# Kernel tuning notes

Measured on AMD Instinct MI355X. Metric: run time of the kernel, lower is better.

## Reference

```python
import jax, jax.numpy as jnp
import numpy as np

B, S, E, H, R = 2, 1024, 1024, 16, 32
D = E // H  # head_dim = 64


def setup_inputs() -> dict:
    key = jax.random.key(0)
    ks = jax.random.split(key, 8)
    f = jax.random.normal
    return {
        "query": f(ks[0], (B, S, E), jnp.float32),
        "key": f(ks[1], (B, S, E), jnp.float32),  # unused by the module's forward, kept for signature fidelity
        "value": f(ks[2], (B, S, E), jnp.float32),
        "rules_keys": f(ks[3], (H, R, D), jnp.float32) * 0.02,   # nn.init.normal_(std=0.02)
        "rules_widths": jnp.ones((H, R, D), jnp.float32),
        "Wq": f(ks[4], (E, E), jnp.float32) * (E ** -0.5),
        "bq": jnp.zeros((E,), jnp.float32),
        "Wv": f(ks[5], (E * R, E), jnp.float32) * (E ** -0.5),
        "bv": jnp.zeros((E * R,), jnp.float32),
        "Wo": f(ks[6], (E, E), jnp.float32) * (E ** -0.5),
        "bo": jnp.zeros((E,), jnp.float32),
    }


def reference(query, key, value, rules_keys, rules_widths, Wq, bq, Wv, bv, Wo, bo):
    scale = D ** -0.5
    # query projection -> per-head layout (B,S,H,D)
    q = ((query @ Wq.T) + bq) * scale
    q = q.reshape(B, S, H, D)
    # fuzzy Gaussian membership: L1 distance to rule keys, scaled by widths,
    # HTSK -> mean over head_dim. z: (B,S,H,R)
    diff = jnp.abs(q[:, :, :, None, :] - rules_keys[None, None])        # (B,S,H,R,D)
    z = -0.5 * jnp.mean((diff / rules_widths[None, None]) ** 2, axis=-1)  # (B,S,H,R)
    attn = jax.nn.softmax(z, axis=-1)  # softmax over rules (dropout p=0 -> identity)
    # value projection to per-rule values: (B,S,H,R,D)
    v = ((value @ Wv.T) + bv) * scale
    v = v.reshape(B, S, H, D, R).transpose(0, 1, 2, 4, 3)
    # rule-weighted aggregation
    out = jnp.einsum('bshr,bshrd->bshd', attn, v)  # (B,S,H,D)
    # faithful to original torch code: transpose(1,2) then view(B,-1,H*D)
    # (this is a head-major flatten, reproduced exactly)
    out = out.transpose(0, 2, 1, 3).reshape(B, S, H * D)
    return (out @ Wo.T) + bo
```

## Files before the change

### kernel.cpp

```cpp
#include <hip/hip_runtime.h>
#include <hip/hip_bf16.h>
#include <cstdint>

typedef float f32x4 __attribute__((ext_vector_type(4)));
typedef short bf16x8 __attribute__((ext_vector_type(8)));

__device__ __forceinline__ unsigned short f32_to_bf16_rne(float f) {
  unsigned int u = __float_as_uint(f);
  return (unsigned short)((u + 0x7FFFu + ((u >> 16) & 1u)) >> 16);
}

#define GLOAD_LDS16(gptr, lptr)                                                             \
  __builtin_amdgcn_global_load_lds((const __attribute__((address_space(1))) unsigned int*)(gptr), \
                                   (__attribute__((address_space(3))) unsigned int*)(lptr), 16, 0, 0)

__global__ __launch_bounds__(256) void cvt_all(const float* __restrict__ wv,
                                               const float* __restrict__ q,
                                               const float* __restrict__ v,
                                               const float* __restrict__ wq,
                                               const float* __restrict__ wo,
                                               unsigned short* __restrict__ wvb,
                                               unsigned short* __restrict__ qb,
                                               unsigned short* __restrict__ vb,
                                               unsigned short* __restrict__ wqb,
                                               unsigned short* __restrict__ wob) {
  int i = blockIdx.x * 256 + threadIdx.x;
  const float* src;
  unsigned short* dst;
  int off;
  if (i < 4194304)      { src = wv; dst = wvb; off = i; }
  else if (i < 4456448) { src = q;  dst = qb;  off = i - 4194304; }
  else if (i < 4718592) { src = v;  dst = vb;  off = i - 4456448; }
  else if (i < 4849664) { src = wq; dst = wqb; off = i - 4718592; }
  else                  { src = wo; dst = wob; off = i - 4849664; }
  const float4* s = (const float4*)src;
  float4 a = s[2 * off], b = s[2 * off + 1];
  uint4 o;
  o.x = (unsigned)f32_to_bf16_rne(a.x) | ((unsigned)f32_to_bf16_rne(a.y) << 16);
  o.y = (unsigned)f32_to_bf16_rne(a.z) | ((unsigned)f32_to_bf16_rne(a.w) << 16);
  o.z = (unsigned)f32_to_bf16_rne(b.x) | ((unsigned)f32_to_bf16_rne(b.y) << 16);
  o.w = (unsigned)f32_to_bf16_rne(b.z) | ((unsigned)f32_to_bf16_rne(b.w) << 16);
  ((uint4*)dst)[off] = o;
}

__global__ __launch_bounds__(256) void fuzzy2_k(const float* __restrict__ qf,
                                                const float* __restrict__ rk,
                                                const float* __restrict__ rw,
                                                float* __restrict__ attn) {
  __shared__ float lk[32][65];
  __shared__ float lc[32][65];
  const int tid = threadIdx.x;
  const int h = blockIdx.y;
  const int mbase = blockIdx.x * 128;

  for (int idx = tid; idx < 2048; idx += 256) {
    int r = idx >> 6, d = idx & 63;
    lk[r][d] = rk[(size_t)(h * 32 + r) * 64 + d];
    float w = rw[(size_t)(h * 32 + r) * 64 + d];
    lc[r][d] = 0.0078125f / (w * w);
  }
  __syncthreads();

  const int g = tid >> 5;
  const int r = tid & 31;
#pragma unroll 1
  for (int it = 0; it < 16; ++it) {
    int m = mbase + it * 8 + g;
    const float* qrow = qf + (size_t)m * 1024 + h * 64;
    float acc = 0.f;
#pragma unroll
    for (int d0 = 0; d0 < 64; d0 += 4) {
      float4 q4 = *(const float4*)(qrow + d0);
      const float* qp = (const float*)&q4;
#pragma unroll
      for (int j = 0; j < 4; ++j) {
        float diff = qp[j] - lk[r][d0 + j];
        acc += lc[r][d0 + j] * diff * diff;
      }
    }
    float z = -acc;
    float mx = z;
#pragma unroll
    for (int mask = 16; mask >= 1; mask >>= 1) mx = fmaxf(mx, __shfl_xor(mx, mask));
    float e = __expf(z - mx);
    float s = e;
#pragma unroll
    for (int mask = 16; mask >= 1; mask >>= 1) s += __shfl_xor(s, mask);
    attn[(size_t)m * 512 + h * 32 + r] = e / s;
  }
}

__global__ __launch_bounds__(256) void gemm_bt64(const unsigned short* __restrict__ A,
                                                 const unsigned short* __restrict__ W,
                                                 const float* __restrict__ bias, float scale,
                                                 int M, int N, int K, float* __restrict__ Cf) {
  constexpr int BK = 32;
  __shared__ unsigned short As[2][64 * BK];
  __shared__ unsigned short Bs[2][64 * BK];
  const int tid = threadIdx.x;
  const int wid = tid >> 6;
  const int lane = tid & 63;
  const int l15 = lane & 15;
  const int l4 = lane >> 4;
  const int bm = blockIdx.y * 64;
  const int bn = blockIdx.x * 64;
  const int wr = (wid >> 1) * 32;
  const int wc = (wid & 1) * 32;

  f32x4 acc[2][2];
#pragma unroll
  for (int i = 0; i < 2; ++i)
#pragma unroll
    for (int j = 0; j < 2; ++j) acc[i][j] = (f32x4){0.f, 0.f, 0.f, 0.f};

  const int nk = K / BK;
  auto stage = [&](int buf, int kt) {
    int c = tid;
    int row = c >> 2, ch = c & 3;
    int sch = ch ^ ((row >> 1) & 3);
    GLOAD_LDS16(A + (size_t)(bm + row) * K + kt * BK + sch * 8, &As[buf][c * 8]);
    GLOAD_LDS16(W + (size_t)(bn + row) * K + kt * BK + sch * 8, &Bs[buf][c * 8]);
  };

  stage(0, 0);
  __syncthreads();

  for (int kt = 0; kt < nk; ++kt) {
    const int cur = kt & 1;
    if (kt + 1 < nk) stage(cur ^ 1, kt + 1);
    bf16x8 a[2], b[2];
#pragma unroll
    for (int mi = 0; mi < 2; ++mi) {
      int rl = wr + mi * 16 + l15;
      int ph = (rl * 64 + l4 * 16) ^ ((((unsigned)rl >> 1) & 3) << 4);
      a[mi] = *(const bf16x8*)((const char*)&As[cur][0] + ph);
    }
#pragma unroll
    for (int ni = 0; ni < 2; ++ni) {
      int rl = wc + ni * 16 + l15;
      int ph = (rl * 64 + l4 * 16) ^ ((((unsigned)rl >> 1) & 3) << 4);
      b[ni] = *(const bf16x8*)((const char*)&Bs[cur][0] + ph);
    }
#pragma unroll
    for (int mi = 0; mi < 2; ++mi)
#pragma unroll
      for (int ni = 0; ni < 2; ++ni)
        acc[mi][ni] = __builtin_amdgcn_mfma_f32_16x16x32_bf16(a[mi], b[ni], acc[mi][ni], 0, 0, 0);
    __syncthreads();
  }

#pragma unroll
  for (int mi = 0; mi < 2; ++mi) {
#pragma unroll
    for (int ni = 0; ni < 2; ++ni) {
      int gm = bm + wr + mi * 16 + l4 * 4;
      int gn = bn + wc + ni * 16 + l15;
      float bval = bias[gn];
#pragma unroll
      for (int q = 0; q < 4; ++q)
        Cf[(size_t)(gm + q) * N + gn] = (acc[mi][ni][q] + bval) * scale;
    }
  }
}

__global__ __launch_bounds__(512, 4) void gemm2_k(const unsigned short* __restrict__ A,
                                                  const unsigned short* __restrict__ W,
                                                  const float* __restrict__ bias, float scale,
                                                  const float* __restrict__ attn,
                                                  unsigned short* __restrict__ X) {
  constexpr int K = 1024, BK = 32, NK = K / BK;
  extern __shared__ unsigned short lds[];
  unsigned short* Asl = lds;
  unsigned short* Bsl = lds + 3 * 4096;
  const int tid = threadIdx.x;
  const int wid = tid >> 6, lane = tid & 63;
  const int l15 = lane & 15, l4 = lane >> 4;
  const int wm = wid >> 2, wn = wid & 3;

  int orig = blockIdx.x;
  int swz = (orig & 7) * 256 + (orig >> 3);
  const int bm = (swz & 15) * 128, bn = (swz >> 4) * 256;

  auto stageA = [&](int buf, int kt) {
    int c = tid;
    int row = c >> 2, ch = c & 3;
    int sch = ch ^ ((row >> 1) & 3);
    GLOAD_LDS16(A + (size_t)(bm + row) * K + kt * BK + sch * 8, Asl + buf * 4096 + c * 8);
  };
  auto stageB = [&](int buf, int kt) {
#pragma unroll
    for (int i = 0; i < 2; ++i) {
      int c = i * 512 + tid;
      int row = c >> 2, ch = c & 3;
      int sch = ch ^ ((row >> 1) & 3);
      GLOAD_LDS16(W + (size_t)(bn + row) * K + kt * BK + sch * 8, Bsl + buf * 8192 + c * 8);
    }
  };

  f32x4 acc[4][4];
#pragma unroll
  for (int i = 0; i < 4; ++i)
#pragma unroll
    for (int j = 0; j < 4; ++j) acc[i][j] = (f32x4){0.f, 0.f, 0.f, 0.f};

  bf16x8 a[4], b[4];

#define FRAG_PH(rl) (((rl) * 64 + l4 * 16) ^ ((((unsigned)(rl) >> 1) & 3) << 4))

#define BODY(CUR, NXT, STG, Tt, DO_STAGE, WN)                                             \
  do {                                                                                    \
    if (DO_STAGE) { stageA(STG, (Tt) + 2); stageB(STG, (Tt) + 2); }                       \
    asm volatile("s_waitcnt vmcnt(" #WN ")" ::: "memory");                                \
    __builtin_amdgcn_s_barrier();                                                         \
    {                                                                                     \
      const char* _ab = (const char*)(Asl + (NXT) * 4096);                                \
      const char* _bb = (const char*)(Bsl + (NXT) * 8192);                                \
      __builtin_amdgcn_s_setprio(1);                                                      \
      _Pragma("unroll") for (int mf = 0; mf < 4; ++mf) {                                  \
        _Pragma("unroll") for (int nf = 0; nf < 4; ++nf) {                                \
          acc[mf][nf] =                                                                   \
              __builtin_amdgcn_mfma_f32_16x16x32_bf16(a[mf], b[nf], acc[mf][nf], 0, 0, 0);\
          if (mf == 3) {                                                                  \
            int rl = wn * 64 + nf * 16 + l15;                                             \
            b[nf] = *(const bf16x8*)(_bb + FRAG_PH(rl));                                  \
          }                                                                               \
        }                                                                                 \
        int rl = wm * 64 + mf * 16 + l15;                                                 \
        a[mf] = *(const bf16x8*)(_ab + FRAG_PH(rl));                                      \
      }                                                                                   \
      __builtin_amdgcn_s_setprio(0);                                                      \
    }                                                                                     \
    asm volatile("s_waitcnt lgkmcnt(0)" ::: "memory");                                    \
    __builtin_amdgcn_sched_barrier(0);                                                    \
  } while (0)

  stageA(0, 0); stageB(0, 0);
  stageA(1, 1); stageB(1, 1);
  asm volatile("s_waitcnt vmcnt(3)" ::: "memory");
  __builtin_amdgcn_s_barrier();
#pragma unroll
  for (int nf = 0; nf < 4; ++nf) {
    int rl = wn * 64 + nf * 16 + l15;
    b[nf] = *(const bf16x8*)((const char*)Bsl + FRAG_PH(rl));
  }
#pragma unroll
  for (int mf = 0; mf < 4; ++mf) {
    int rl = wm * 64 + mf * 16 + l15;
    a[mf] = *(const bf16x8*)((const char*)Asl + FRAG_PH(rl));
  }
  asm volatile("s_waitcnt lgkmcnt(0)" ::: "memory");
  __builtin_amdgcn_sched_barrier(0);

  for (int T = 0; T < 30; T += 3) {
    BODY(0, 1, 2, T, 1, 3);
    BODY(1, 2, 0, (T + 1), 1, 3);
    BODY(2, 0, 1, (T + 2), 1, 3);
  }
  BODY(0, 1, 2, 30, 0, 0);
  __builtin_amdgcn_s_setprio(1);
#pragma unroll
  for (int mf = 0; mf < 4; ++mf)
#pragma unroll
    for (int nf = 0; nf < 4; ++nf)
      acc[mf][nf] = __builtin_amdgcn_mfma_f32_16x16x32_bf16(a[mf], b[nf], acc[mf][nf], 0, 0, 0);
  __builtin_amdgcn_s_setprio(0);
#undef BODY
#undef FRAG_PH

  const int h = bn >> 11;
  const int dbase = ((bn & 2047) + wn * 64) >> 5;
#pragma unroll
  for (int mf = 0; mf < 4; ++mf) {
    int gm0 = bm + wm * 64 + mf * 16 + l4 * 4;
    float red[4][2];
#pragma unroll
    for (int q = 0; q < 4; ++q) { red[q][0] = 0.f; red[q][1] = 0.f; }
#pragma unroll
    for (int nf = 0; nf < 4; ++nf) {
      int col = bn + wn * 64 + nf * 16 + l15;
      float bval = bias[col];
      int r = (nf & 1) * 16 + l15;
      int g = nf >> 1;
#pragma unroll
      for (int q = 0; q < 4; ++q) {
        float w = attn[(size_t)(gm0 + q) * 512 + h * 32 + r];
        red[q][g] += (acc[mf][nf][q] + bval) * w;
      }
    }
#pragma unroll
    for (int q = 0; q < 4; ++q)
#pragma unroll
      for (int g = 0; g < 2; ++g) {
        float vv = red[q][g];
        for (int mask = 1; mask < 16; mask <<= 1) vv += __shfl_xor(vv, mask);
        red[q][g] = vv * scale;
      }
    if (l15 == 0) {
#pragma unroll
      for (int q = 0; q < 4; ++q) {
        int m = gm0 + q;
        int bb = m >> 10, s = m & 1023;
        size_t base = (((size_t)(bb * 16 + h)) * 1024 + s) * 64;
        unsigned lo = f32_to_bf16_rne(red[q][0]);
        unsigned hi = f32_to_bf16_rne(red[q][1]);
        ((unsigned*)X)[(base + dbase) >> 1] = lo | (hi << 16);
      }
    }
  }
}

extern "C" void kernel_launch(void* const* d_in, const int* in_sizes, int n_in, void* d_out,
                              int out_size, void* d_ws, size_t ws_size, hipStream_t stream) {
  const float* query = (const float*)d_in[0];
  const float* value = (const float*)d_in[2];
  const float* rk = (const float*)d_in[3];
  const float* rw = (const float*)d_in[4];
  const float* Wq = (const float*)d_in[5];
  const float* bq = (const float*)d_in[6];
  const float* Wv = (const float*)d_in[7];
  const float* bv = (const float*)d_in[8];
  const float* Wo = (const float*)d_in[9];
  const float* bo = (const float*)d_in[10];
  float* out = (float*)d_out;

  const float scale = 0.125f;

  char* p = (char*)d_ws;
  unsigned short* Wv_b = (unsigned short*)p; p += (size_t)33554432 * 2;
  unsigned short* Aq_b = (unsigned short*)p; p += (size_t)2097152 * 2;
  unsigned short* Av_b = (unsigned short*)p; p += (size_t)2097152 * 2;
  unsigned short* Wq_b = (unsigned short*)p; p += (size_t)1048576 * 2;
  unsigned short* Wo_b = (unsigned short*)p; p += (size_t)1048576 * 2;
  float* qf = (float*)p;   p += (size_t)2097152 * 4;
  float* attn = (float*)p; p += (size_t)1048576 * 4;
  unsigned short* X = (unsigned short*)p;

  cvt_all<<<19456, 256, 0, stream>>>(Wv, query, value, Wq, Wo, Wv_b, Aq_b, Av_b, Wq_b, Wo_b);

  gemm_bt64<<<dim3(16, 32), 256, 0, stream>>>(Aq_b, Wq_b, bq, scale, 2048, 1024, 1024, qf);
  fuzzy2_k<<<dim3(16, 16), 256, 0, stream>>>(qf, rk, rw, attn);
  hipFuncSetAttribute((const void*)gemm2_k, hipFuncAttributeMaxDynamicSharedMemorySize, 73728);
  gemm2_k<<<2048, 512, 73728, stream>>>(Av_b, Wv_b, bv, scale, attn, X);
  gemm_bt64<<<dim3(16, 32), 256, 0, stream>>>(X, Wo_b, bo, 1.0f, 2048, 1024, 1024, out);
}
```

Before: 235.2 us.

## Enlarge gemm2 tile to 256x256 with 4-stage LDS ring and double-buffered fragments

```diff
diff --git a/kernel.cpp b/kernel.cpp
--- a/kernel.cpp
+++ b/kernel.cpp
@@ -163,29 +163,32 @@
   }
 }
 
-__global__ __launch_bounds__(512, 4) void gemm2_k(const unsigned short* __restrict__ A,
-                                                  const unsigned short* __restrict__ W,
-                                                  const float* __restrict__ bias, float scale,
-                                                  const float* __restrict__ attn,
-                                                  unsigned short* __restrict__ X) {
+__global__ __launch_bounds__(512) void gemm2_k(const unsigned short* __restrict__ A,
+                                               const unsigned short* __restrict__ W,
+                                               const float* __restrict__ bias, float scale,
+                                               const float* __restrict__ attn,
+                                               unsigned short* __restrict__ X) {
   constexpr int K = 1024, BK = 32, NK = K / BK;
   extern __shared__ unsigned short lds[];
   unsigned short* Asl = lds;
-  unsigned short* Bsl = lds + 3 * 4096;
+  unsigned short* Bsl = lds + 4 * 8192;
   const int tid = threadIdx.x;
   const int wid = tid >> 6, lane = tid & 63;
   const int l15 = lane & 15, l4 = lane >> 4;
   const int wm = wid >> 2, wn = wid & 3;
 
   int orig = blockIdx.x;
-  int swz = (orig & 7) * 256 + (orig >> 3);
-  const int bm = (swz & 15) * 128, bn = (swz >> 4) * 256;
+  int swz = (orig & 7) * 128 + (orig >> 3);
+  const int bm = (swz & 7) * 256, bn = (swz >> 3) * 256;
 
   auto stageA = [&](int buf, int kt) {
-    int c = tid;
-    int row = c >> 2, ch = c & 3;
-    int sch = ch ^ ((row >> 1) & 3);
-    GLOAD_LDS16(A + (size_t)(bm + row) * K + kt * BK + sch * 8, Asl + buf * 4096 + c * 8);
+#pragma unroll
+    for (int i = 0; i < 2; ++i) {
+      int c = i * 512 + tid;
+      int row = c >> 2, ch = c & 3;
+      int sch = ch ^ ((row >> 1) & 3);
+      GLOAD_LDS16(A + (size_t)(bm + row) * K + kt * BK + sch * 8, Asl + buf * 8192 + c * 8);
+    }
   };
   auto stageB = [&](int buf, int kt) {
 #pragma unroll
@@ -197,36 +200,37 @@
     }
   };
 
-  f32x4 acc[4][4];
-#pragma unroll
-  for (int i = 0; i < 4; ++i)
+  f32x4 acc[8][4];
+#pragma unroll
+  for (int i = 0; i < 8; ++i)
 #pragma unroll
     for (int j = 0; j < 4; ++j) acc[i][j] = (f32x4){0.f, 0.f, 0.f, 0.f};
 
-  bf16x8 a[4], b[4];
+  bf16x8 a0[8], a1[8], b0[4], b1[4];
 
 #define FRAG_PH(rl) (((rl) * 64 + l4 * 16) ^ ((((unsigned)(rl) >> 1) & 3) << 4))
 
-#define BODY(CUR, NXT, STG, Tt, DO_STAGE, WN)                                             \
+#define BODY(aC, aN, bC, bN, Tt, DO_STAGE, WN)                                            \
   do {                                                                                    \
-    if (DO_STAGE) { stageA(STG, (Tt) + 2); stageB(STG, (Tt) + 2); }                       \
+    if (DO_STAGE) { stageA(((Tt) + 2) & 3, (Tt) + 2); stageB(((Tt) + 2) & 3, (Tt) + 2); } \
     asm volatile("s_waitcnt vmcnt(" #WN ")" ::: "memory");                                \
     __builtin_amdgcn_s_barrier();                                                         \
     {                                                                                     \
-      const char* _ab = (const char*)(Asl + (NXT) * 4096);                                \
-      const char* _bb = (const char*)(Bsl + (NXT) * 8192);                                \
+      const char* _ab = (const char*)(Asl + (((Tt) + 1) & 3) * 8192);                     \
+      const char* _bb = (const char*)(Bsl + (((Tt) + 1) & 3) * 8192);                     \
       __builtin_amdgcn_s_setprio(1);                                                      \
-      _Pragma("unroll") for (int mf = 0; mf < 4; ++mf) {                                  \
-        _Pragma("unroll") for (int nf = 0; nf < 4; ++nf) {                                \
+      _Pragma("unroll") for (int mf = 0; mf < 8; ++mf) {                                  \
+        _Pragma("unroll") for (int nf = 0; nf < 4; ++nf)                                  \
           acc[mf][nf] =                                                                   \
-              __builtin_amdgcn_mfma_f32_16x16x32_bf16(a[mf], b[nf], acc[mf][nf], 0, 0, 0);\
-          if (mf == 3) {                                                                  \
-            int rl = wn * 64 + nf * 16 + l15;                                             \
-            b[nf] = *(const bf16x8*)(_bb + FRAG_PH(rl));                                  \
-          }                                                                               \
+              __builtin_amdgcn_mfma_f32_16x16x32_bf16(aC[mf], bC[nf], acc[mf][nf], 0, 0, 0); \
+        if (mf < 4) {                                                                     \
+          aN[mf] = *(const bf16x8*)(_ab + FRAG_PH(wm * 128 + mf * 16 + l15));             \
+          bN[mf] = *(const bf16x8*)(_bb + FRAG_PH(wn * 64 + mf * 16 + l15));              \
+        } else if (mf < 6) {                                                              \
+          int i0 = 2 * mf - 4, i1 = 2 * mf - 3;                                           \
+          aN[i0] = *(const bf16x8*)(_ab + FRAG_PH(wm * 128 + i0 * 16 + l15));             \
+          aN[i1] = *(const bf16x8*)(_ab + FRAG_PH(wm * 128 + i1 * 16 + l15));             \
         }                                                                                 \
-        int rl = wm * 64 + mf * 16 + l15;                                                 \
-        a[mf] = *(const bf16x8*)(_ab + FRAG_PH(rl));                                      \
       }                                                                                   \
       __builtin_amdgcn_s_setprio(0);                                                      \
     }                                                                                     \
@@ -236,33 +240,28 @@
 
   stageA(0, 0); stageB(0, 0);
   stageA(1, 1); stageB(1, 1);
-  asm volatile("s_waitcnt vmcnt(3)" ::: "memory");
+  asm volatile("s_waitcnt vmcnt(4)" ::: "memory");
   __builtin_amdgcn_s_barrier();
 #pragma unroll
-  for (int nf = 0; nf < 4; ++nf) {
-    int rl = wn * 64 + nf * 16 + l15;
-    b[nf] = *(const bf16x8*)((const char*)Bsl + FRAG_PH(rl));
-  }
-#pragma unroll
-  for (int mf = 0; mf < 4; ++mf) {
-    int rl = wm * 64 + mf * 16 + l15;
-    a[mf] = *(const bf16x8*)((const char*)Asl + FRAG_PH(rl));
-  }
+  for (int nf = 0; nf < 4; ++nf)
+    b0[nf] = *(const bf16x8*)((const char*)Bsl + FRAG_PH(wn * 64 + nf * 16 + l15));
+#pragma unroll
+  for (int mf = 0; mf < 8; ++mf)
+    a0[mf] = *(const bf16x8*)((const char*)Asl + FRAG_PH(wm * 128 + mf * 16 + l15));
   asm volatile("s_waitcnt lgkmcnt(0)" ::: "memory");
   __builtin_amdgcn_sched_barrier(0);
 
-  for (int T = 0; T < 30; T += 3) {
-    BODY(0, 1, 2, T, 1, 3);
-    BODY(1, 2, 0, (T + 1), 1, 3);
-    BODY(2, 0, 1, (T + 2), 1, 3);
-  }
-  BODY(0, 1, 2, 30, 0, 0);
+  for (int T = 0; T < 30; T += 2) {
+    BODY(a0, a1, b0, b1, T, 1, 4);
+    BODY(a1, a0, b1, b0, (T + 1), 1, 4);
+  }
+  BODY(a0, a1, b0, b1, 30, 0, 0);
   __builtin_amdgcn_s_setprio(1);
 #pragma unroll
-  for (int mf = 0; mf < 4; ++mf)
+  for (int mf = 0; mf < 8; ++mf)
 #pragma unroll
     for (int nf = 0; nf < 4; ++nf)
-      acc[mf][nf] = __builtin_amdgcn_mfma_f32_16x16x32_bf16(a[mf], b[nf], acc[mf][nf], 0, 0, 0);
+      acc[mf][nf] = __builtin_amdgcn_mfma_f32_16x16x32_bf16(a1[mf], b1[nf], acc[mf][nf], 0, 0, 0);
   __builtin_amdgcn_s_setprio(0);
 #undef BODY
 #undef FRAG_PH
@@ -270,8 +269,8 @@
   const int h = bn >> 11;
   const int dbase = ((bn & 2047) + wn * 64) >> 5;
 #pragma unroll
-  for (int mf = 0; mf < 4; ++mf) {
-    int gm0 = bm + wm * 64 + mf * 16 + l4 * 4;
+  for (int mf = 0; mf < 8; ++mf) {
+    int gm0 = bm + wm * 128 + mf * 16 + l4 * 4;
     float red[4][2];
 #pragma unroll
     for (int q = 0; q < 4; ++q) { red[q][0] = 0.f; red[q][1] = 0.f; }
@@ -339,7 +338,7 @@
 
   gemm_bt64<<<dim3(16, 32), 256, 0, stream>>>(Aq_b, Wq_b, bq, scale, 2048, 1024, 1024, qf);
   fuzzy2_k<<<dim3(16, 16), 256, 0, stream>>>(qf, rk, rw, attn);
-  hipFuncSetAttribute((const void*)gemm2_k, hipFuncAttributeMaxDynamicSharedMemorySize, 73728);
-  gemm2_k<<<2048, 512, 73728, stream>>>(Av_b, Wv_b, bv, scale, attn, X);
+  hipFuncSetAttribute((const void*)gemm2_k, hipFuncAttributeMaxDynamicSharedMemorySize, 131072);
+  gemm2_k<<<1024, 512, 131072, stream>>>(Av_b, Wv_b, bv, scale, attn, X);
   gemm_bt64<<<dim3(16, 32), 256, 0, stream>>>(X, Wo_b, bo, 1.0f, 2048, 1024, 1024, out);
 }
```

Measured after the change: 232.0 us. No clear change (-1.4%).
